# Optimization experiments

Hardware: AMD Instinct MI355X
Metric: run time of the kernel (lower is better)

Reference implementation:

```python
import jax, jax.numpy as jnp
from jax import lax
import numpy as np

B, T, I, H, O = 512, 2048, 8, 128, 96


def setup_inputs() -> dict:
    key = jax.random.key(0)
    ks = jax.random.split(key, 7)
    s = 1.0 / np.sqrt(H)  # PyTorch GRU init scale
    return {
        "x": jax.random.normal(ks[0], (B, T, I), dtype=jnp.float32),
        "w_ih": jax.random.uniform(ks[1], (3 * H, I), jnp.float32, -s, s),
        "w_hh": jax.random.uniform(ks[2], (3 * H, H), jnp.float32, -s, s),
        "b_ih": jax.random.uniform(ks[3], (3 * H,), jnp.float32, -s, s),
        "b_hh": jax.random.uniform(ks[4], (3 * H,), jnp.float32, -s, s),
        "fc_w": jax.random.uniform(ks[5], (O, H), jnp.float32, -s, s),
        "fc_b": jax.random.uniform(ks[6], (O,), jnp.float32, -s, s),
    }


def reference(x, w_ih, w_hh, b_ih, b_hh, fc_w, fc_b):
    # x: [B, T, I]; PyTorch GRU gate order: reset, update, new (r, z, n)
    Bh, Th, _ = x.shape
    Hh = w_hh.shape[1]
    # Precompute input contributions for all timesteps in one big GEMM.
    gx_all = jnp.einsum('bti,gi->btg', x, w_ih) + b_ih      # [B, T, 3H]
    gx_all = jnp.swapaxes(gx_all, 0, 1)                     # [T, B, 3H]

    def step(h, gx):
        gh = h @ w_hh.T + b_hh                              # [B, 3H]
        r = jax.nn.sigmoid(gx[:, :Hh] + gh[:, :Hh])
        z = jax.nn.sigmoid(gx[:, Hh:2 * Hh] + gh[:, Hh:2 * Hh])
        n = jnp.tanh(gx[:, 2 * Hh:] + r * gh[:, 2 * Hh:])
        h_new = (1.0 - z) * n + z * h
        return h_new, None

    h0 = jnp.zeros((Bh, Hh), x.dtype)
    h_last, _ = lax.scan(step, h0, gx_all)                  # h at final timestep
    return h_last @ fc_w.T + fc_b                           # [B, O]
```

## Files before the change

### kernel.cpp

```cpp
#include <hip/hip_runtime.h>

#define BB 512
#define TT 2048
#define II 8
#define HH 128
#define OO 96

typedef __attribute__((ext_vector_type(8))) short bf16x8;
typedef __attribute__((ext_vector_type(4))) float f32x4;

#define L2E 1.4426950408889634f

__device__ __forceinline__ float fast_rcp(float x) { return __builtin_amdgcn_rcpf(x); }
__device__ __forceinline__ float exp2_fast(float x) {
#if __has_builtin(__builtin_amdgcn_exp2f)
    return __builtin_amdgcn_exp2f(x);
#else
    return __expf(x * 0.6931471805599453f);
#endif
}
__device__ __forceinline__ unsigned short f2bf(float f) {
    unsigned int u = __builtin_bit_cast(unsigned int, f);
    u += 0x7fffu + ((u >> 16) & 1u);
    return (unsigned short)(u >> 16);
}
__device__ __forceinline__ float bf2f(unsigned short h) {
    unsigned int u = ((unsigned int)h) << 16;
    return __builtin_bit_cast(float, u);
}
__device__ __forceinline__ float dot8(const float w[8], float4 a, float4 b, float acc) {
    acc = fmaf(w[0], a.x, acc); acc = fmaf(w[1], a.y, acc);
    acc = fmaf(w[2], a.z, acc); acc = fmaf(w[3], a.w, acc);
    acc = fmaf(w[4], b.x, acc); acc = fmaf(w[5], b.y, acc);
    acc = fmaf(w[6], b.z, acc); acc = fmaf(w[7], b.w, acc);
    return acc;
}

__global__ __launch_bounds__(256, 1) void gru_kernel(
    const float* __restrict__ x,
    const float* __restrict__ w_ih,
    const float* __restrict__ w_hh,
    const float* __restrict__ b_ih,
    const float* __restrict__ b_hh,
    const float* __restrict__ fc_w,
    const float* __restrict__ fc_b,
    float* __restrict__ out)
{
    __shared__ __align__(16) char hbuf[2 * 1280];
    __shared__ __align__(16) float hfin[2][HH];

    const int tid = threadIdx.x;
    const int wv  = tid >> 6;
    const int ln  = tid & 63;
    const int col = ln & 15;
    const int g4  = ln >> 4;
    const int b   = g4 & 1;
    const int sel = g4 >> 1;
    const int p   = ((ln >> 2) & 1) * 2 + (ln & 1);
    const int jA  = 32 * wv + col;
    const int jB  = jA + 16;
    const int jS  = jA + 16 * sel;
    const int b0  = blockIdx.x * 2;

    auto ldfrag_hh = [&](int grow, int ks, float sc) {
        const float* rowp = w_hh + grow * HH + 32 * ks + g4 * 8;
        float4 u = *(const float4*)(rowp);
        float4 v = *(const float4*)(rowp + 4);
        bf16x8 f;
        f[0] = (short)f2bf(sc * u.x); f[1] = (short)f2bf(sc * u.y);
        f[2] = (short)f2bf(sc * u.z); f[3] = (short)f2bf(sc * u.w);
        f[4] = (short)f2bf(sc * v.x); f[5] = (short)f2bf(sc * v.y);
        f[6] = (short)f2bf(sc * v.z); f[7] = (short)f2bf(sc * v.w);
        return f;
    };

    bf16x8 bRA[4], bZA[4], bNA[4], bRB[4], bZB[4], bNB[4];
#pragma unroll
    for (int ks = 0; ks < 4; ++ks) {
        bRA[ks] = ldfrag_hh(jA, ks, -L2E);
        bZA[ks] = ldfrag_hh(HH + jA, ks, -L2E);
        bNA[ks] = ldfrag_hh(2 * HH + jA, ks, 2.0f * L2E);
        bRB[ks] = ldfrag_hh(jB, ks, -L2E);
        bZB[ks] = ldfrag_hh(HH + jB, ks, -L2E);
        bNB[ks] = ldfrag_hh(2 * HH + jB, ks, 2.0f * L2E);
    }

    float wr[8], wz[8], wn[8];
    {
        const float* r0p = w_ih + jS * II;
        const float* r1p = w_ih + (HH + jS) * II;
        const float* r2p = w_ih + (2 * HH + jS) * II;
#pragma unroll
        for (int i = 0; i < 8; ++i) {
            wr[i] = -L2E * r0p[i];
            wz[i] = -L2E * r1p[i];
            wn[i] = (2.0f * L2E) * r2p[i];
        }
    }

    const float bias_r2  = -L2E * (b_ih[jS] + b_hh[jS]);
    const float bias_z2  = -L2E * (b_ih[HH + jS] + b_hh[HH + jS]);
    const float bias_nh2 = (2.0f * L2E) * b_hh[2 * HH + jS];
    const float bias_nx2 = (2.0f * L2E) * b_ih[2 * HH + jS];

    for (int i = tid; i < 640; i += 256) ((int*)hbuf)[i] = 0;
    __syncthreads();

    const char* abase = hbuf + p * 320 + g4 * 16;
    char* wbase = hbuf + b * 640 + (jS << 1);
    const float* xp = x + (size_t)(b0 + b) * TT * II;

    float h0 = 0.f;

    float gxr0, gxz0, gxn0, gxr1, gxz1, gxn1;
    {
        float4 xa = *(const float4*)(xp);          float4 xb = *(const float4*)(xp + 4);
        float4 xc = *(const float4*)(xp + II);     float4 xd = *(const float4*)(xp + II + 4);
        gxr0 = dot8(wr, xa, xb, bias_r2);  gxz0 = dot8(wz, xa, xb, bias_z2);  gxn0 = dot8(wn, xa, xb, bias_nx2);
        gxr1 = dot8(wr, xc, xd, bias_r2);  gxz1 = dot8(wz, xc, xd, bias_z2);  gxn1 = dot8(wn, xc, xd, bias_nx2);
    }
    float gxr0n, gxz0n, gxn0n, gxr1n, gxz1n, gxn1n;

#define MFMA_BF16 __builtin_amdgcn_mfma_f32_16x16x32_bf16

#define STEP(RBUF, GXR, GXZ, GXN, DOTS)                                         \
    {                                                                           \
        const char* ab = abase + (RBUF) * 1280;                                 \
        bf16x8 a0 = *(const bf16x8*)(ab);                                       \
        bf16x8 a1 = *(const bf16x8*)(ab + 64);                                  \
        bf16x8 a2 = *(const bf16x8*)(ab + 128);                                 \
        bf16x8 a3 = *(const bf16x8*)(ab + 192);                                 \
        f32x4 aRA = {(GXR), 0.f, 0.f, 0.f};                                     \
        f32x4 aZA = {(GXZ), 0.f, 0.f, 0.f};                                     \
        f32x4 aNA = {bias_nh2, 0.f, 0.f, 0.f};                                  \
        f32x4 aRB = {(GXR), 0.f, 0.f, 0.f};                                     \
        f32x4 aZB = {(GXZ), 0.f, 0.f, 0.f};                                     \
        f32x4 aNB = {bias_nh2, 0.f, 0.f, 0.f};                                  \
        float gxn_ = (GXN);                                                     \
        aRA = MFMA_BF16(a0, bRA[0], aRA, 0, 0, 0);                              \
        aZA = MFMA_BF16(a0, bZA[0], aZA, 0, 0, 0);                              \
        aNA = MFMA_BF16(a0, bNA[0], aNA, 0, 0, 0);                              \
        aRB = MFMA_BF16(a0, bRB[0], aRB, 0, 0, 0);                              \
        aZB = MFMA_BF16(a0, bZB[0], aZB, 0, 0, 0);                              \
        aNB = MFMA_BF16(a0, bNB[0], aNB, 0, 0, 0);                              \
        aRA = MFMA_BF16(a1, bRA[1], aRA, 0, 0, 0);                              \
        aZA = MFMA_BF16(a1, bZA[1], aZA, 0, 0, 0);                              \
        aNA = MFMA_BF16(a1, bNA[1], aNA, 0, 0, 0);                              \
        aRB = MFMA_BF16(a1, bRB[1], aRB, 0, 0, 0);                              \
        aZB = MFMA_BF16(a1, bZB[1], aZB, 0, 0, 0);                              \
        aNB = MFMA_BF16(a1, bNB[1], aNB, 0, 0, 0);                              \
        aRA = MFMA_BF16(a2, bRA[2], aRA, 0, 0, 0);                              \
        aZA = MFMA_BF16(a2, bZA[2], aZA, 0, 0, 0);                              \
        aNA = MFMA_BF16(a2, bNA[2], aNA, 0, 0, 0);                              \
        aRB = MFMA_BF16(a2, bRB[2], aRB, 0, 0, 0);                              \
        aZB = MFMA_BF16(a2, bZB[2], aZB, 0, 0, 0);                              \
        aNB = MFMA_BF16(a2, bNB[2], aNB, 0, 0, 0);                              \
        aRA = MFMA_BF16(a3, bRA[3], aRA, 0, 0, 0);                              \
        aZA = MFMA_BF16(a3, bZA[3], aZA, 0, 0, 0);                              \
        aNA = MFMA_BF16(a3, bNA[3], aNA, 0, 0, 0);                              \
        aRB = MFMA_BF16(a3, bRB[3], aRB, 0, 0, 0);                              \
        aZB = MFMA_BF16(a3, bZB[3], aZB, 0, 0, 0);                              \
        aNB = MFMA_BF16(a3, bNB[3], aNB, 0, 0, 0);                              \
        DOTS                                                                    \
        float grA = aRA[0] + aRA[1], grB = aRB[0] + aRB[1];                     \
        float gzA = aZA[0] + aZA[1], gzB = aZB[0] + aZB[1];                     \
        float gnA = aNA[0] + aNA[1], gnB = aNB[0] + aNB[1];                     \
        float gr = sel ? grB : grA;                                             \
        float gz = sel ? gzB : gzA;                                             \
        float gn = sel ? gnB : gnA;                                             \
        float r0 = fast_rcp(1.0f + exp2_fast(gr));                              \
        float z0 = fast_rcp(1.0f + exp2_fast(gz));                              \
        float t0 = fast_rcp(1.0f + exp2_fast(fmaf(r0, gn, gxn_)));              \
        float n0 = fmaf(-2.0f, t0, 1.0f);                                       \
        h0 = fmaf(z0, h0 - n0, n0);                                             \
        {                                                                       \
            char* w_ = wbase + (1 - (RBUF)) * 1280;                             \
            unsigned short s0 = f2bf(h0);                                       \
            *(unsigned short*)(w_)       = s0;                                  \
            *(unsigned short*)(w_ + 320) = f2bf(h0 - bf2f(s0));                 \
        }                                                                       \
        __syncthreads();                                                        \
    }

    for (int it = 0; it < TT / 2; ++it) {
        int t2 = 2 * it + 2; if (t2 > TT - 1) t2 = TT - 1;
        int t3 = t2 + 1;     if (t3 > TT - 1) t3 = TT - 1;
        float4 pa = *(const float4*)(xp + (size_t)t2 * II);
        float4 pb = *(const float4*)(xp + (size_t)t2 * II + 4);
        float4 pc = *(const float4*)(xp + (size_t)t3 * II);
        float4 pd = *(const float4*)(xp + (size_t)t3 * II + 4);

        STEP(0, gxr0, gxz0, gxn0, {})
        STEP(1, gxr1, gxz1, gxn1, {
            gxr0n = dot8(wr, pa, pb, bias_r2);
            gxz0n = dot8(wz, pa, pb, bias_z2);
            gxn0n = dot8(wn, pa, pb, bias_nx2);
            gxr1n = dot8(wr, pc, pd, bias_r2);
            gxz1n = dot8(wz, pc, pd, bias_z2);
            gxn1n = dot8(wn, pc, pd, bias_nx2);
        })
        gxr0 = gxr0n; gxz0 = gxz0n; gxn0 = gxn0n;
        gxr1 = gxr1n; gxz1 = gxz1n; gxn1 = gxn1n;
    }
#undef STEP
#undef MFMA_BF16

    hfin[b][jS] = h0;
    __syncthreads();

    if (tid < 2 * OO) {
        const int bb2 = (tid >= OO) ? 1 : 0;
        const int o   = tid - OO * bb2;
        const float4* hf = (const float4*)(&hfin[bb2][0]);
        const float4* wp = (const float4*)(fc_w + o * HH);
        float acc = fc_b[o];
#pragma unroll 8
        for (int v = 0; v < HH / 4; ++v) {
            float4 w4 = wp[v];
            float4 h4 = hf[v];
            acc = fmaf(w4.x, h4.x, acc); acc = fmaf(w4.y, h4.y, acc);
            acc = fmaf(w4.z, h4.z, acc); acc = fmaf(w4.w, h4.w, acc);
        }
        out[(size_t)(b0 + bb2) * OO + o] = acc;
    }
}

extern "C" void kernel_launch(void* const* d_in, const int* in_sizes, int n_in,
                              void* d_out, int out_size, void* d_ws, size_t ws_size,
                              hipStream_t stream) {
    const float* x    = (const float*)d_in[0];
    const float* w_ih = (const float*)d_in[1];
    const float* w_hh = (const float*)d_in[2];
    const float* b_ih = (const float*)d_in[3];
    const float* b_hh = (const float*)d_in[4];
    const float* fc_w = (const float*)d_in[5];
    const float* fc_b = (const float*)d_in[6];
    float* out = (float*)d_out;

    gru_kernel<<<BB / 2, 256, 0, stream>>>(x, w_ih, w_hh, b_ih, b_hh, fc_w, fc_b, out);
}
```

Baseline: 1.105 ms.

## Split hidden units across eight waves and use a lighter step barrier

Doubles the block to 512 threads so each wave owns 16 hidden columns instead of 32. Each wave now issues 12 MFMAs per step instead of 24, and the per-lane select between the A and B halves goes away. The block-wide __syncthreads is replaced by an explicit lgkmcnt wait plus s_barrier to cut barrier overhead. The trade-off is a barrier across twice as many waves on a latency-bound recurrence, and redundant lanes now write the same h values to shared memory.

After: 1.054 ms. 4.6% less time.

```diff
diff --git a/kernel.cpp b/kernel.cpp
--- a/kernel.cpp
+++ b/kernel.cpp
@@ -36,7 +36,7 @@
     return acc;
 }
 
-__global__ __launch_bounds__(256, 1) void gru_kernel(
+__global__ __launch_bounds__(512, 2) void gru_kernel(
     const float* __restrict__ x,
     const float* __restrict__ w_ih,
     const float* __restrict__ w_hh,
@@ -55,11 +55,8 @@
     const int col = ln & 15;
     const int g4  = ln >> 4;
     const int b   = g4 & 1;
-    const int sel = g4 >> 1;
     const int p   = ((ln >> 2) & 1) * 2 + (ln & 1);
-    const int jA  = 32 * wv + col;
-    const int jB  = jA + 16;
-    const int jS  = jA + 16 * sel;
+    const int j   = 16 * wv + col;
     const int b0  = blockIdx.x * 2;
 
     auto ldfrag_hh = [&](int grow, int ks, float sc) {
@@ -74,22 +71,19 @@
         return f;
     };
 
-    bf16x8 bRA[4], bZA[4], bNA[4], bRB[4], bZB[4], bNB[4];
+    bf16x8 bR[4], bZ[4], bN[4];
 #pragma unroll
     for (int ks = 0; ks < 4; ++ks) {
-        bRA[ks] = ldfrag_hh(jA, ks, -L2E);
-        bZA[ks] = ldfrag_hh(HH + jA, ks, -L2E);
-        bNA[ks] = ldfrag_hh(2 * HH + jA, ks, 2.0f * L2E);
-        bRB[ks] = ldfrag_hh(jB, ks, -L2E);
-        bZB[ks] = ldfrag_hh(HH + jB, ks, -L2E);
-        bNB[ks] = ldfrag_hh(2 * HH + jB, ks, 2.0f * L2E);
+        bR[ks] = ldfrag_hh(j, ks, -L2E);
+        bZ[ks] = ldfrag_hh(HH + j, ks, -L2E);
+        bN[ks] = ldfrag_hh(2 * HH + j, ks, 2.0f * L2E);
     }
 
     float wr[8], wz[8], wn[8];
     {
-        const float* r0p = w_ih + jS * II;
-        const float* r1p = w_ih + (HH + jS) * II;
-        const float* r2p = w_ih + (2 * HH + jS) * II;
+        const float* r0p = w_ih + j * II;
+        const float* r1p = w_ih + (HH + j) * II;
+        const float* r2p = w_ih + (2 * HH + j) * II;
 #pragma unroll
         for (int i = 0; i < 8; ++i) {
             wr[i] = -L2E * r0p[i];
@@ -98,16 +92,16 @@
         }
     }
 
-    const float bias_r2  = -L2E * (b_ih[jS] + b_hh[jS]);
-    const float bias_z2  = -L2E * (b_ih[HH + jS] + b_hh[HH + jS]);
-    const float bias_nh2 = (2.0f * L2E) * b_hh[2 * HH + jS];
-    const float bias_nx2 = (2.0f * L2E) * b_ih[2 * HH + jS];
-
-    for (int i = tid; i < 640; i += 256) ((int*)hbuf)[i] = 0;
+    const float bias_r2  = -L2E * (b_ih[j] + b_hh[j]);
+    const float bias_z2  = -L2E * (b_ih[HH + j] + b_hh[HH + j]);
+    const float bias_nh2 = (2.0f * L2E) * b_hh[2 * HH + j];
+    const float bias_nx2 = (2.0f * L2E) * b_ih[2 * HH + j];
+
+    for (int i = tid; i < 640; i += 512) ((int*)hbuf)[i] = 0;
     __syncthreads();
 
     const char* abase = hbuf + p * 320 + g4 * 16;
-    char* wbase = hbuf + b * 640 + (jS << 1);
+    char* wbase = hbuf + b * 640 + (j << 1);
     const float* xp = x + (size_t)(b0 + b) * TT * II;
 
     float h0 = 0.f;
@@ -122,6 +116,11 @@
     float gxr0n, gxz0n, gxn0n, gxr1n, gxz1n, gxn1n;
 
 #define MFMA_BF16 __builtin_amdgcn_mfma_f32_16x16x32_bf16
+
+#define STEP_BARRIER()                                                          \
+    asm volatile("s_waitcnt lgkmcnt(0)" ::: "memory");                          \
+    __builtin_amdgcn_s_barrier();                                               \
+    asm volatile("" ::: "memory");
 
 #define STEP(RBUF, GXR, GXZ, GXN, DOTS)                                         \
     {                                                                           \
@@ -130,47 +129,28 @@
         bf16x8 a1 = *(const bf16x8*)(ab + 64);                                  \
         bf16x8 a2 = *(const bf16x8*)(ab + 128);                                 \
         bf16x8 a3 = *(const bf16x8*)(ab + 192);                                 \
-        f32x4 aRA = {(GXR), 0.f, 0.f, 0.f};                                     \
-        f32x4 aZA = {(GXZ), 0.f, 0.f, 0.f};                                     \
-        f32x4 aNA = {bias_nh2, 0.f, 0.f, 0.f};                                  \
-        f32x4 aRB = {(GXR), 0.f, 0.f, 0.f};                                     \
-        f32x4 aZB = {(GXZ), 0.f, 0.f, 0.f};                                     \
-        f32x4 aNB = {bias_nh2, 0.f, 0.f, 0.f};                                  \
-        float gxn_ = (GXN);                                                     \
-        aRA = MFMA_BF16(a0, bRA[0], aRA, 0, 0, 0);                              \
-        aZA = MFMA_BF16(a0, bZA[0], aZA, 0, 0, 0);                              \
-        aNA = MFMA_BF16(a0, bNA[0], aNA, 0, 0, 0);                              \
-        aRB = MFMA_BF16(a0, bRB[0], aRB, 0, 0, 0);                              \
-        aZB = MFMA_BF16(a0, bZB[0], aZB, 0, 0, 0);                              \
-        aNB = MFMA_BF16(a0, bNB[0], aNB, 0, 0, 0);                              \
-        aRA = MFMA_BF16(a1, bRA[1], aRA, 0, 0, 0);                              \
-        aZA = MFMA_BF16(a1, bZA[1], aZA, 0, 0, 0);                              \
-        aNA = MFMA_BF16(a1, bNA[1], aNA, 0, 0, 0);                              \
-        aRB = MFMA_BF16(a1, bRB[1], aRB, 0, 0, 0);                              \
-        aZB = MFMA_BF16(a1, bZB[1], aZB, 0, 0, 0);                              \
-        aNB = MFMA_BF16(a1, bNB[1], aNB, 0, 0, 0);                              \
-        aRA = MFMA_BF16(a2, bRA[2], aRA, 0, 0, 0);                              \
-        aZA = MFMA_BF16(a2, bZA[2], aZA, 0, 0, 0);                              \
-        aNA = MFMA_BF16(a2, bNA[2], aNA, 0, 0, 0);                              \
-        aRB = MFMA_BF16(a2, bRB[2], aRB, 0, 0, 0);                              \
-        aZB = MFMA_BF16(a2, bZB[2], aZB, 0, 0, 0);                              \
-        aNB = MFMA_BF16(a2, bNB[2], aNB, 0, 0, 0);                              \
-        aRA = MFMA_BF16(a3, bRA[3], aRA, 0, 0, 0);                              \
-        aZA = MFMA_BF16(a3, bZA[3], aZA, 0, 0, 0);                              \
-        aNA = MFMA_BF16(a3, bNA[3], aNA, 0, 0, 0);                              \
-        aRB = MFMA_BF16(a3, bRB[3], aRB, 0, 0, 0);                              \
-        aZB = MFMA_BF16(a3, bZB[3], aZB, 0, 0, 0);                              \
-        aNB = MFMA_BF16(a3, bNB[3], aNB, 0, 0, 0);                              \
+        f32x4 aR = {(GXR), 0.f, 0.f, 0.f};                                      \
+        f32x4 aZ = {(GXZ), 0.f, 0.f, 0.f};                                      \
+        f32x4 aN = {bias_nh2, 0.f, 0.f, 0.f};                                   \
+        aR = MFMA_BF16(a0, bR[0], aR, 0, 0, 0);                                 \
+        aZ = MFMA_BF16(a0, bZ[0], aZ, 0, 0, 0);                                 \
+        aN = MFMA_BF16(a0, bN[0], aN, 0, 0, 0);                                 \
+        aR = MFMA_BF16(a1, bR[1], aR, 0, 0, 0);                                 \
+        aZ = MFMA_BF16(a1, bZ[1], aZ, 0, 0, 0);                                 \
+        aN = MFMA_BF16(a1, bN[1], aN, 0, 0, 0);                                 \
+        aR = MFMA_BF16(a2, bR[2], aR, 0, 0, 0);                                 \
+        aZ = MFMA_BF16(a2, bZ[2], aZ, 0, 0, 0);                                 \
+        aN = MFMA_BF16(a2, bN[2], aN, 0, 0, 0);                                 \
+        aR = MFMA_BF16(a3, bR[3], aR, 0, 0, 0);                                 \
+        aZ = MFMA_BF16(a3, bZ[3], aZ, 0, 0, 0);                                 \
+        aN = MFMA_BF16(a3, bN[3], aN, 0, 0, 0);                                 \
         DOTS                                                                    \
-        float grA = aRA[0] + aRA[1], grB = aRB[0] + aRB[1];                     \
-        float gzA = aZA[0] + aZA[1], gzB = aZB[0] + aZB[1];                     \
-        float gnA = aNA[0] + aNA[1], gnB = aNB[0] + aNB[1];                     \
-        float gr = sel ? grB : grA;                                             \
-        float gz = sel ? gzB : gzA;                                             \
-        float gn = sel ? gnB : gnA;                                             \
+        float gr = aR[0] + aR[1];                                               \
+        float gz = aZ[0] + aZ[1];                                               \
+        float gn = aN[0] + aN[1];                                               \
         float r0 = fast_rcp(1.0f + exp2_fast(gr));                              \
         float z0 = fast_rcp(1.0f + exp2_fast(gz));                              \
-        float t0 = fast_rcp(1.0f + exp2_fast(fmaf(r0, gn, gxn_)));              \
+        float t0 = fast_rcp(1.0f + exp2_fast(fmaf(r0, gn, (GXN))));             \
         float n0 = fmaf(-2.0f, t0, 1.0f);                                       \
         h0 = fmaf(z0, h0 - n0, n0);                                             \
         {                                                                       \
@@ -179,7 +159,7 @@
             *(unsigned short*)(w_)       = s0;                                  \
             *(unsigned short*)(w_ + 320) = f2bf(h0 - bf2f(s0));                 \
         }                                                                       \
-        __syncthreads();                                                        \
+        STEP_BARRIER()                                                          \
     }
 
     for (int it = 0; it < TT / 2; ++it) {
@@ -203,9 +183,10 @@
         gxr1 = gxr1n; gxz1 = gxz1n; gxn1 = gxn1n;
     }
 #undef STEP
+#undef STEP_BARRIER
 #undef MFMA_BF16
 
-    hfin[b][jS] = h0;
+    if (ln < 32) hfin[b][j] = h0;
     __syncthreads();
 
     if (tid < 2 * OO) {
@@ -237,5 +218,5 @@
     const float* fc_b = (const float*)d_in[6];
     float* out = (float*)d_out;
 
-    gru_kernel<<<BB / 2, 256, 0, stream>>>(x, w_ih, w_hh, b_ih, b_hh, fc_w, fc_b, out);
-}
+    gru_kernel<<<BB / 2, 512, 0, stream>>>(x, w_ih, w_hh, b_ih, b_hh, fc_w, fc_b, out);
+}
```
